# Kernel tuning notes

Hardware: AMD Instinct MI355X
Metric: run time of the kernel (lower is better)

Reference implementation:

```python
import jax, jax.numpy as jnp
import numpy as np


def dense_image_warp(image, flow):
    """Faithful port of tfa.image.dense_image_warp.
    query(y,x) = grid(y,x) - flow(y,x); bilinear sample with floor clipped to
    [0, size-2] and alpha clipped to [0,1] (matches tfa _interpolate_bilinear 'ij').
    image: [B,H,W,C] float, flow: [B,H,W,2] float -> [B,H,W,C]
    """
    B, H, W, C = image.shape
    gy = jnp.arange(H, dtype=flow.dtype)
    gx = jnp.arange(W, dtype=flow.dtype)
    grid = jnp.stack(jnp.meshgrid(gy, gx, indexing='ij'), axis=-1)  # [H,W,2]
    query = grid[None] - flow  # [B,H,W,2]
    qy, qx = query[..., 0], query[..., 1]
    fy = jnp.clip(jnp.floor(qy), 0.0, H - 2)
    fx = jnp.clip(jnp.floor(qx), 0.0, W - 2)
    ay = jnp.clip(qy - fy, 0.0, 1.0)[..., None]  # [B,H,W,1]
    ax = jnp.clip(qx - fx, 0.0, 1.0)[..., None]
    y0 = fy.astype(jnp.int32)
    x0 = fx.astype(jnp.int32)
    b = jnp.arange(B)[:, None, None]
    tl = image[b, y0, x0]
    tr = image[b, y0, x0 + 1]
    bl = image[b, y0 + 1, x0]
    br = image[b, y0 + 1, x0 + 1]
    top = tl + ax * (tr - tl)
    bot = bl + ax * (br - bl)
    return top + ay * (bot - top)


def setup_inputs() -> dict:
    key = jax.random.key(0)
    ks = jax.random.split(key, 6)
    B, H, W, C = 16, 512, 512, 3
    return {
        'frame_0': jax.random.uniform(ks[0], (B, H, W, C), jnp.float32),
        'frame_1': jax.random.uniform(ks[1], (B, H, W, C), jnp.float32),
        'f_01': jax.random.normal(ks[2], (B, H, W, 2), jnp.float32) * 5.0,
        'f_10': jax.random.normal(ks[3], (B, H, W, 2), jnp.float32) * 5.0,
        'f_t0': jax.random.normal(ks[4], (B, H, W, 2), jnp.float32) * 5.0,
        'f_t1': jax.random.normal(ks[5], (B, H, W, 2), jnp.float32) * 5.0,
    }


def reference(frame_0, frame_1, f_01, f_10, f_t0, f_t1):
    return (
        dense_image_warp(frame_1, f_01),
        dense_image_warp(frame_0, f_10),
        dense_image_warp(frame_0, f_t0),
        dense_image_warp(frame_1, f_t1),
    )
```

## Files before the change

### kernel.cpp

```cpp
#include <hip/hip_runtime.h>

#define HH 512
#define WW 512
#define NPIX (16 * HH * WW)
#define IMG_DW (HH * WW * 3)
#define ROWD_G (WW * 3)

#define TSX   32
#define TSY   16
#define APRX  12
#define APRY  10
#define LWX   (TSX + 2 * APRX)
#define LWY   (TSY + 2 * APRY)
#define ROWD  (LWX * 3)
#define LSTR  172
#define LDSDW (LWY * LSTR)
#define NCHUNK (LDSDW / 4)

typedef float fv4 __attribute__((ext_vector_type(4)));
typedef float fv2 __attribute__((ext_vector_type(2)));
typedef fv4 fv4u __attribute__((aligned(4)));
typedef fv2 fv2u __attribute__((aligned(4)));

__device__ __forceinline__ void sample(const float* __restrict__ imgb,
                                       const float* __restrict__ s,
                                       int AX0, int AY0,
                                       float qy, float qx, float* __restrict__ r)
{
    float fy = floorf(qy); fy = fminf(fmaxf(fy, 0.0f), (float)(HH - 2));
    float fx = floorf(qx); fx = fminf(fmaxf(fx, 0.0f), (float)(WW - 2));
    const float ay = fminf(fmaxf(qy - fy, 0.0f), 1.0f);
    const float ax = fminf(fmaxf(qx - fx, 0.0f), 1.0f);
    const int y0 = (int)fy, x0 = (int)fx;
    const int yl = y0 - AY0, xl = x0 - AX0;
    if ((unsigned)yl < (unsigned)(LWY - 1) && (unsigned)xl < (unsigned)(LWX - 1)) {
        const float* t  = s + yl * LSTR + 3 * xl;
        const float* bo = t + LSTR;
#pragma unroll
        for (int c = 0; c < 3; ++c) {
            const float tl = t[c],  tr = t[c + 3];
            const float bl = bo[c], br = bo[c + 3];
            const float top = tl + ax * (tr - tl);
            const float bot = bl + ax * (br - bl);
            r[c] = top + ay * (bot - top);
        }
    } else {
        const float* t  = imgb + ((size_t)y0 * WW + x0) * 3;
        const float* bo = t + WW * 3;
        const fv4u t4 = *(const fv4u*)t;  const fv2u t2 = *(const fv2u*)(t + 4);
        const fv4u b4 = *(const fv4u*)bo; const fv2u b2 = *(const fv2u*)(bo + 4);
        const float tv[6] = {t4.x, t4.y, t4.z, t4.w, t2.x, t2.y};
        const float bv[6] = {b4.x, b4.y, b4.z, b4.w, b2.x, b2.y};
#pragma unroll
        for (int c = 0; c < 3; ++c) {
            const float top = tv[c] + ax * (tv[c + 3] - tv[c]);
            const float bot = bv[c] + ax * (bv[c + 3] - bv[c]);
            r[c] = top + ay * (bot - top);
        }
    }
}

__global__ __launch_bounds__(256) void warp_glds6_kernel(
    const float* __restrict__ frame0, const float* __restrict__ frame1,
    const float* __restrict__ f01, const float* __restrict__ f10,
    const float* __restrict__ ft0, const float* __restrict__ ft1,
    float* __restrict__ out)
{
    __shared__ float lds[LDSDW];

    const unsigned bid = blockIdx.x;
    const unsigned v   = (bid & 7u) * 2048u + (bid >> 3);

    const unsigned tile  = v & 511u;
    const unsigned img_b = v >> 9;
    const int b  = (int)(img_b & 15u);
    const int fg = (int)(img_b >> 4);

    const int tx = (int)(tile & 15u);
    const int ty = (int)(tile >> 4);
    const int X0 = tx * TSX, Y0 = ty * TSY;
    const int AX0 = X0 - APRX, AY0 = Y0 - APRY;

    const float* img   = fg ? frame1 : frame0;
    const float* flowA = fg ? f01 : f10;
    const float* flowB = fg ? ft1 : ft0;
    const size_t opA   = fg ? 0 : 1;
    const size_t opB   = fg ? 3 : 2;

    const float* imgb = img + (size_t)b * IMG_DW;

    const int tid = (int)threadIdx.x;
    const int lx = (tid & 15) * 2;
    const int ly = tid >> 4;
    const int x = X0 + lx, y = Y0 + ly;
    const size_t pixIn = ((size_t)b * HH + y) * WW + x;

    const fv4 a = __builtin_nontemporal_load((const fv4*)(flowA + pixIn * 2));
    const fv4 c = __builtin_nontemporal_load((const fv4*)(flowB + pixIn * 2));

    {
        const unsigned wid = __builtin_amdgcn_readfirstlane((unsigned)tid >> 6);
        int D   = tid * 4;
        int row = D / LSTR;
        int rd  = D - row * LSTR;
#pragma unroll
        for (int it = 0; it < 7; ++it) {
            if (it < 6 || tid < (NCHUNK - 6 * 256)) {
                const int gy = min(max(AY0 + row, 0), HH - 1);
                int idx = gy * ROWD_G + AX0 * 3 + rd;
                idx = min(max(idx, 0), IMG_DW - 4);
                const float* src = imgb + idx;
                float* dst = (float*)lds + it * 1024 + wid * 256;
                __builtin_amdgcn_global_load_lds(
                    (const __attribute__((address_space(1))) void*)src,
                    (__attribute__((address_space(3))) void*)dst, 16, 0, 0);
            }
            row += 5; rd += 164;
            if (rd >= LSTR) { rd -= LSTR; ++row; }
        }
    }
    __syncthreads();

    float* oA = out + (opA * NPIX + pixIn) * 3;
    float* oB = out + (opB * NPIX + pixIn) * 3;

    {
        float res[6];
        sample(imgb, lds, AX0, AY0, (float)y - a.x, (float)x       - a.y, res);
        sample(imgb, lds, AX0, AY0, (float)y - a.z, (float)(x + 1) - a.w, res + 3);
        fv2 v0s = {res[0], res[1]};
        fv2 v1s = {res[2], res[3]};
        fv2 v2s = {res[4], res[5]};
        __builtin_nontemporal_store(v0s, (fv2*)oA);
        __builtin_nontemporal_store(v1s, (fv2*)oA + 1);
        __builtin_nontemporal_store(v2s, (fv2*)oA + 2);
    }
    {
        float res[6];
        sample(imgb, lds, AX0, AY0, (float)y - c.x, (float)x       - c.y, res);
        sample(imgb, lds, AX0, AY0, (float)y - c.z, (float)(x + 1) - c.w, res + 3);
        fv2 v0s = {res[0], res[1]};
        fv2 v1s = {res[2], res[3]};
        fv2 v2s = {res[4], res[5]};
        __builtin_nontemporal_store(v0s, (fv2*)oB);
        __builtin_nontemporal_store(v1s, (fv2*)oB + 1);
        __builtin_nontemporal_store(v2s, (fv2*)oB + 2);
    }
}

extern "C" void kernel_launch(void* const* d_in, const int* in_sizes, int n_in,
                              void* d_out, int out_size, void* d_ws, size_t ws_size,
                              hipStream_t stream) {
    const float* frame0 = (const float*)d_in[0];
    const float* frame1 = (const float*)d_in[1];
    const float* f01    = (const float*)d_in[2];
    const float* f10    = (const float*)d_in[3];
    const float* ft0    = (const float*)d_in[4];
    const float* ft1    = (const float*)d_in[5];
    float* out = (float*)d_out;

    hipLaunchKernelGGL(warp_glds6_kernel, dim3(16384), dim3(256), 0, stream,
                       frame0, frame1, f01, f10, ft0, ft1, out);
}
```

Baseline: 98.07 us.

## Double-buffer LDS tiles so each block processes four x-tiles with prefetch

```diff
diff --git a/kernel.cpp b/kernel.cpp
--- a/kernel.cpp
+++ b/kernel.cpp
@@ -16,11 +16,34 @@
 #define LSTR  172
 #define LDSDW (LWY * LSTR)
 #define NCHUNK (LDSDW / 4)
+#define NTILE 4
 
 typedef float fv4 __attribute__((ext_vector_type(4)));
 typedef float fv2 __attribute__((ext_vector_type(2)));
 typedef fv4 fv4u __attribute__((aligned(4)));
 typedef fv2 fv2u __attribute__((aligned(4)));
+
+__device__ __forceinline__ void stage(const float* __restrict__ imgb,
+                                      float* __restrict__ ldsbase,
+                                      int AX0, int AY0, int tid, unsigned wid)
+{
+    int row = (tid * 4) / LSTR;
+    int rd  = (tid * 4) - row * LSTR;
+#pragma unroll
+    for (int it = 0; it < 7; ++it) {
+        if (it < 6 || tid < (NCHUNK - 6 * 256)) {
+            const int gy = min(max(AY0 + row, 0), HH - 1);
+            int idx = gy * ROWD_G + AX0 * 3 + rd;
+            idx = min(max(idx, 0), IMG_DW - 4);
+            __builtin_amdgcn_global_load_lds(
+                (const __attribute__((address_space(1))) void*)(imgb + idx),
+                (__attribute__((address_space(3))) void*)(ldsbase + it * 1024 + wid * 256),
+                16, 0, 0);
+        }
+        row += 5; rd += 164;
+        if (rd >= LSTR) { rd -= LSTR; ++row; }
+    }
+}
 
 __device__ __forceinline__ void sample(const float* __restrict__ imgb,
                                        const float* __restrict__ s,
@@ -60,91 +83,89 @@
     }
 }
 
-__global__ __launch_bounds__(256) void warp_glds6_kernel(
+__global__ __launch_bounds__(256) void warp_dbuf_kernel(
     const float* __restrict__ frame0, const float* __restrict__ frame1,
     const float* __restrict__ f01, const float* __restrict__ f10,
     const float* __restrict__ ft0, const float* __restrict__ ft1,
     float* __restrict__ out)
 {
-    __shared__ float lds[LDSDW];
+    __shared__ float lds[2 * LDSDW];
 
     const unsigned bid = blockIdx.x;
-    const unsigned v   = (bid & 7u) * 2048u + (bid >> 3);
+    const unsigned u   = (bid & 7u) * 512u + (bid >> 3);
 
-    const unsigned tile  = v & 511u;
-    const unsigned img_b = v >> 9;
+    const int ux    = (int)(u & 3u);
+    const int ty    = (int)((u >> 2) & 31u);
+    const unsigned img_b = u >> 7;
     const int b  = (int)(img_b & 15u);
     const int fg = (int)(img_b >> 4);
 
-    const int tx = (int)(tile & 15u);
-    const int ty = (int)(tile >> 4);
-    const int X0 = tx * TSX, Y0 = ty * TSY;
-    const int AX0 = X0 - APRX, AY0 = Y0 - APRY;
+    const int txb = ux * NTILE;
+    const int Y0  = ty * TSY;
+    const int AY0 = Y0 - APRY;
 
     const float* img   = fg ? frame1 : frame0;
     const float* flowA = fg ? f01 : f10;
     const float* flowB = fg ? ft1 : ft0;
     const size_t opA   = fg ? 0 : 1;
     const size_t opB   = fg ? 3 : 2;
-
-    const float* imgb = img + (size_t)b * IMG_DW;
+    const float* imgb  = img + (size_t)b * IMG_DW;
 
     const int tid = (int)threadIdx.x;
+    const unsigned wid = __builtin_amdgcn_readfirstlane((unsigned)tid >> 6);
     const int lx = (tid & 15) * 2;
     const int ly = tid >> 4;
-    const int x = X0 + lx, y = Y0 + ly;
-    const size_t pixIn = ((size_t)b * HH + y) * WW + x;
+    const int y  = Y0 + ly;
+    const size_t rowBase = ((size_t)b * HH + y) * WW;
 
-    const fv4 a = __builtin_nontemporal_load((const fv4*)(flowA + pixIn * 2));
-    const fv4 c = __builtin_nontemporal_load((const fv4*)(flowB + pixIn * 2));
+    stage(imgb, lds, txb * TSX - APRX, AY0, tid, wid);
+    fv4 fa = __builtin_nontemporal_load((const fv4*)(flowA + (rowBase + txb * TSX + lx) * 2));
+    fv4 fc = __builtin_nontemporal_load((const fv4*)(flowB + (rowBase + txb * TSX + lx) * 2));
 
-    {
-        const unsigned wid = __builtin_amdgcn_readfirstlane((unsigned)tid >> 6);
-        int D   = tid * 4;
-        int row = D / LSTR;
-        int rd  = D - row * LSTR;
 #pragma unroll
-        for (int it = 0; it < 7; ++it) {
-            if (it < 6 || tid < (NCHUNK - 6 * 256)) {
-                const int gy = min(max(AY0 + row, 0), HH - 1);
-                int idx = gy * ROWD_G + AX0 * 3 + rd;
-                idx = min(max(idx, 0), IMG_DW - 4);
-                const float* src = imgb + idx;
-                float* dst = (float*)lds + it * 1024 + wid * 256;
-                __builtin_amdgcn_global_load_lds(
-                    (const __attribute__((address_space(1))) void*)src,
-                    (__attribute__((address_space(3))) void*)dst, 16, 0, 0);
-            }
-            row += 5; rd += 164;
-            if (rd >= LSTR) { rd -= LSTR; ++row; }
+    for (int t = 0; t < NTILE; ++t) {
+        const int X0  = (txb + t) * TSX;
+        const int AX0 = X0 - APRX;
+        const int x   = X0 + lx;
+        const size_t pixIn = rowBase + x;
+
+        __syncthreads();
+
+        fv4 fa_n = fa, fc_n = fc;
+        if (t < NTILE - 1) {
+            stage(imgb, lds + ((t + 1) & 1) * LDSDW, AX0 + TSX, AY0, tid, wid);
+            fa_n = __builtin_nontemporal_load((const fv4*)(flowA + (pixIn + TSX) * 2));
+            fc_n = __builtin_nontemporal_load((const fv4*)(flowB + (pixIn + TSX) * 2));
         }
-    }
-    __syncthreads();
 
-    float* oA = out + (opA * NPIX + pixIn) * 3;
-    float* oB = out + (opB * NPIX + pixIn) * 3;
+        const float* sbuf = lds + (t & 1) * LDSDW;
+        float* oA = out + (opA * NPIX + pixIn) * 3;
+        float* oB = out + (opB * NPIX + pixIn) * 3;
 
-    {
-        float res[6];
-        sample(imgb, lds, AX0, AY0, (float)y - a.x, (float)x       - a.y, res);
-        sample(imgb, lds, AX0, AY0, (float)y - a.z, (float)(x + 1) - a.w, res + 3);
-        fv2 v0s = {res[0], res[1]};
-        fv2 v1s = {res[2], res[3]};
-        fv2 v2s = {res[4], res[5]};
-        __builtin_nontemporal_store(v0s, (fv2*)oA);
-        __builtin_nontemporal_store(v1s, (fv2*)oA + 1);
-        __builtin_nontemporal_store(v2s, (fv2*)oA + 2);
-    }
-    {
-        float res[6];
-        sample(imgb, lds, AX0, AY0, (float)y - c.x, (float)x       - c.y, res);
-        sample(imgb, lds, AX0, AY0, (float)y - c.z, (float)(x + 1) - c.w, res + 3);
-        fv2 v0s = {res[0], res[1]};
-        fv2 v1s = {res[2], res[3]};
-        fv2 v2s = {res[4], res[5]};
-        __builtin_nontemporal_store(v0s, (fv2*)oB);
-        __builtin_nontemporal_store(v1s, (fv2*)oB + 1);
-        __builtin_nontemporal_store(v2s, (fv2*)oB + 2);
+        {
+            float res[6];
+            sample(imgb, sbuf, AX0, AY0, (float)y - fa.x, (float)x       - fa.y, res);
+            sample(imgb, sbuf, AX0, AY0, (float)y - fa.z, (float)(x + 1) - fa.w, res + 3);
+            fv2 v0s = {res[0], res[1]};
+            fv2 v1s = {res[2], res[3]};
+            fv2 v2s = {res[4], res[5]};
+            __builtin_nontemporal_store(v0s, (fv2*)oA);
+            __builtin_nontemporal_store(v1s, (fv2*)oA + 1);
+            __builtin_nontemporal_store(v2s, (fv2*)oA + 2);
+        }
+        {
+            float res[6];
+            sample(imgb, sbuf, AX0, AY0, (float)y - fc.x, (float)x       - fc.y, res);
+            sample(imgb, sbuf, AX0, AY0, (float)y - fc.z, (float)(x + 1) - fc.w, res + 3);
+            fv2 v0s = {res[0], res[1]};
+            fv2 v1s = {res[2], res[3]};
+            fv2 v2s = {res[4], res[5]};
+            __builtin_nontemporal_store(v0s, (fv2*)oB);
+            __builtin_nontemporal_store(v1s, (fv2*)oB + 1);
+            __builtin_nontemporal_store(v2s, (fv2*)oB + 2);
+        }
+
+        fa = fa_n; fc = fc_n;
     }
 }
 
@@ -159,6 +180,6 @@
     const float* ft1    = (const float*)d_in[5];
     float* out = (float*)d_out;
 
-    hipLaunchKernelGGL(warp_glds6_kernel, dim3(16384), dim3(256), 0, stream,
+    hipLaunchKernelGGL(warp_dbuf_kernel, dim3(4096), dim3(256), 0, stream,
                        frame0, frame1, f01, f10, ft0, ft1, out);
 }
```

Result: slower. 105.5 us (+7.5%).
